# Kernel optimization log

Hardware: AMD Instinct MI355X
Metric: run time of the kernel (lower is better)

Reference implementation:

```python
import jax, jax.numpy as jnp
import numpy as np

B, C, N = 4, 256, 4096
QK = 32  # query/key channel dim hardcoded in module


def setup_inputs() -> dict:
    key = jax.random.key(0)
    ks = jax.random.split(key, 5)
    sc = 1.0 / np.sqrt(C)
    return {
        "x": jax.random.normal(ks[0], (B, C, N), dtype=jnp.float32),
        "Wf": jax.random.normal(ks[1], (QK, C), dtype=jnp.float32) * sc,
        "bf": jnp.zeros((QK,), dtype=jnp.float32),
        "Wg": jax.random.normal(ks[2], (QK, C), dtype=jnp.float32) * sc,
        "bg": jnp.zeros((QK,), dtype=jnp.float32),
        "Wh": jax.random.normal(ks[3], (C, C), dtype=jnp.float32) * sc,
        "bh": jnp.zeros((C,), dtype=jnp.float32),
        "gamma": jax.random.normal(ks[4], (1,), dtype=jnp.float32) * 0.1,
    }


def reference(x, Wf, bf, Wg, bg, Wh, bh, gamma):
    # 1x1 Conv1d == channel-mixing matmul: (O,C) x (B,C,N) -> (B,O,N)
    f = jnp.einsum('oc,bcn->bon', Wf, x) + bf[:, None]   # (B, 32, N)
    g = jnp.einsum('oc,bcn->bon', Wg, x) + bg[:, None]   # (B, 32, N)
    h = jnp.einsum('oc,bcn->bon', Wh, x) + bh[:, None]   # (B, C, N)
    # attention[b, n, m] = sum_k f[b,k,n] * g[b,k,m]  (unscaled, per source)
    attn = jax.nn.softmax(jnp.einsum('bkn,bkm->bnm', f, g), axis=-1)  # (B,N,N)
    # torch.bmm(h, attention): out[b,c,m] = sum_n h[b,c,n] * attn[b,n,m]
    sa = jnp.einsum('bcn,bnm->bcm', h, attn)             # (B, C, N)
    return gamma * sa + x
```

## Files before the change

kernel.cpp:

```cpp
#include <hip/hip_runtime.h>
#include <hip/hip_bf16.h>
#include <math.h>

constexpr int Bb = 4;
constexpr int Cc = 256;
constexpr int Nn = 4096;
constexpr int K  = 32;

constexpr float LOG2E = 1.4426950408889634f;
constexpr float C40L  = 40.0f * LOG2E;

typedef __attribute__((ext_vector_type(8))) short short8;
typedef __attribute__((ext_vector_type(4))) float f32x4;
typedef __attribute__((ext_vector_type(2))) unsigned int uint2v;

static __device__ __forceinline__ unsigned int pack2(float a, float b) {
  union { __hip_bfloat162 h2; unsigned int u; } cv;
  cv.h2 = __float22bfloat162_rn(float2{a, b});
  return cv.u;
}
static __device__ __forceinline__ unsigned short f2bf(float f) {
  union { __hip_bfloat16 h; unsigned short u; } cv;
  cv.h = __float2bfloat16(f);
  return cv.u;
}
static __device__ __forceinline__ f32x4 MF(short8 a, short8 b, f32x4 c) {
  return __builtin_amdgcn_mfma_f32_16x16x32_bf16(a, b, c, 0, 0, 0);
}
static __device__ __forceinline__ float ex2(float v) {
  return __builtin_amdgcn_exp2f(v);
}
static __device__ __forceinline__ void stage16(const unsigned short* g,
                                               unsigned short* l) {
  __builtin_amdgcn_global_load_lds(
      (const __attribute__((address_space(1))) unsigned int*)g,
      (__attribute__((address_space(3))) unsigned int*)l, 16, 0, 0);
}


__global__ __launch_bounds__(256) void castW(
    const float* __restrict__ Wh, unsigned short* __restrict__ Whb)
{
  int i = (blockIdx.x * 256 + threadIdx.x) * 4;
  float4 v = *(const float4*)&Wh[i];
  uint2 o = { pack2(v.x, v.y), pack2(v.z, v.w) };
  *(uint2*)&Whb[i] = o;
}

__global__ __launch_bounds__(256) void castFG(
    const float* __restrict__ Wf, const float* __restrict__ Wg,
    unsigned short* __restrict__ Wfgb)
{
  int g = (blockIdx.x * 256 + threadIdx.x) * 4;
  int row = g >> 8, c = g & 255;
  const float* src = (row < 32) ? &Wf[row*Cc + c] : &Wg[(row-32)*Cc + c];
  float4 v = *(const float4*)src;
  uint2 o = { pack2(v.x, v.y), pack2(v.z, v.w) };
  *(uint2*)&Wfgb[g] = o;
}

__global__ __launch_bounds__(256) void trans_k(
    const float* __restrict__ x, unsigned short* __restrict__ xT)
{
  __shared__ unsigned short Ls[64][65];
  const int b  = blockIdx.z;
  const int n0 = blockIdx.x * 64, c0 = blockIdx.y * 64;
  const int tid = threadIdx.x;
  {
    const int cr = tid >> 4, n4 = (tid & 15) * 4;
#pragma unroll
    for (int rr = 0; rr < 4; ++rr) {
      int c = rr * 16 + cr;
      float4 v = *(const float4*)&x[(size_t)(b*Cc + c0 + c)*Nn + n0 + n4];
      Ls[c][n4+0] = f2bf(v.x); Ls[c][n4+1] = f2bf(v.y);
      Ls[c][n4+2] = f2bf(v.z); Ls[c][n4+3] = f2bf(v.w);
    }
  }
  __syncthreads();
  {
    const int nw = tid >> 4, cw = (tid & 15) * 4;
#pragma unroll
    for (int rr = 0; rr < 4; ++rr) {
      int n = nw + rr * 16;
      unsigned int lo = (unsigned int)Ls[cw+0][n] | ((unsigned int)Ls[cw+1][n] << 16);
      unsigned int hi = (unsigned int)Ls[cw+2][n] | ((unsigned int)Ls[cw+3][n] << 16);
      uint2 o = { lo, hi };
      *(uint2*)&xT[(size_t)(b*Nn + n0 + n)*Cc + c0 + cw] = o;
    }
  }
}

__global__ __launch_bounds__(256) void proj_fgM(
    const unsigned short* __restrict__ xT, const unsigned short* __restrict__ Wfgb,
    const float* __restrict__ bf, const float* __restrict__ bg,
    unsigned short* __restrict__ Ft, unsigned short* __restrict__ Gt)
{
  const int b = blockIdx.y;
  const int tid = threadIdx.x, wave = tid >> 6, lane = tid & 63;
  const int q = lane >> 4, col = lane & 15;
  const int n = blockIdx.x * 64 + wave * 16 + col;

  const unsigned short* Bp = xT + (size_t)(b*Nn + n)*Cc + q*8;
  const f32x4 zero = {0.f,0.f,0.f,0.f};
  f32x4 af0 = zero, af1 = zero, ag0 = zero, ag1 = zero;
#pragma unroll
  for (int kc = 0; kc < 8; ++kc) {
    short8 bn = *(const short8*)(Bp + kc*32);
    short8 a0 = *(const short8*)(Wfgb + (size_t)( 0 + col)*Cc + kc*32 + q*8);
    short8 a1 = *(const short8*)(Wfgb + (size_t)(16 + col)*Cc + kc*32 + q*8);
    short8 a2 = *(const short8*)(Wfgb + (size_t)(32 + col)*Cc + kc*32 + q*8);
    short8 a3 = *(const short8*)(Wfgb + (size_t)(48 + col)*Cc + kc*32 + q*8);
    af0 = MF(a0, bn, af0); af1 = MF(a1, bn, af1);
    ag0 = MF(a2, bn, ag0); ag1 = MF(a3, bn, ag1);
  }
  float4 bf0 = *(const float4*)&bf[q*4],      bf1 = *(const float4*)&bf[16 + q*4];
  float4 bg0 = *(const float4*)&bg[q*4],      bg1 = *(const float4*)&bg[16 + q*4];
  uint2 F0 = { pack2((af0[0]+bf0.x)*LOG2E, (af0[1]+bf0.y)*LOG2E),
               pack2((af0[2]+bf0.z)*LOG2E, (af0[3]+bf0.w)*LOG2E) };
  uint2 F1 = { pack2((af1[0]+bf1.x)*LOG2E, (af1[1]+bf1.y)*LOG2E),
               pack2((af1[2]+bf1.z)*LOG2E, (af1[3]+bf1.w)*LOG2E) };
  uint2 G0 = { pack2(ag0[0]+bg0.x, ag0[1]+bg0.y), pack2(ag0[2]+bg0.z, ag0[3]+bg0.w) };
  uint2 G1 = { pack2(ag1[0]+bg1.x, ag1[1]+bg1.y), pack2(ag1[2]+bg1.z, ag1[3]+bg1.w) };
  unsigned short* fo = Ft + (size_t)(b*Nn + n)*K;
  unsigned short* go = Gt + (size_t)(b*Nn + n)*K;
  *(uint2*)(fo + q*4) = F0;  *(uint2*)(fo + 16 + q*4) = F1;
  *(uint2*)(go + q*4) = G0;  *(uint2*)(go + 16 + q*4) = G1;
}

__global__ __launch_bounds__(512) void pass1(
    const unsigned short* __restrict__ Ft, const unsigned short* __restrict__ Gt,
    unsigned short* __restrict__ Et, float* __restrict__ Lp)
{
  __shared__ float red[8][64];
  const int n0 = blockIdx.x * 64;
  const int mh = blockIdx.y;
  const int b  = blockIdx.z;
  const int tid = threadIdx.x, wave = tid >> 6, lane = tid & 63;
  const int q = lane >> 4, col = lane & 15;
  const unsigned short* Fb = Ft + (size_t)b*Nn*K;
  const unsigned short* Gb = Gt + (size_t)b*Nn*K;
  unsigned short* Ebt = Et + (size_t)b*Nn*Nn;

  short8 af[4];
#pragma unroll
  for (int rb = 0; rb < 4; ++rb)
    af[rb] = *(const short8*)(Fb + (size_t)(n0 + rb*16 + col)*K + q*8);

  const int mw = mh*2048 + wave*256;
  const f32x4 cinit = {-C40L, -C40L, -C40L, -C40L};
  float l[16];
#pragma unroll
  for (int i = 0; i < 16; ++i) l[i] = 0.f;

  unsigned short* sbase = Ebt + (size_t)(n0 >> 3)*128
                        + (q >> 1)*128 + col*8 + (q & 1)*4;

  short8 gA = *(const short8*)(Gb + (size_t)(mw + col)*K + q*8);
  for (int it = 0; it < 16; ++it) {
    short8 gB = *(const short8*)(Gb + (size_t)(mw + ((it+1)&15)*16 + col)*K + q*8);
    f32x4 ts[4];
    ts[0] = MF(af[0], gA, cinit);
    ts[1] = MF(af[1], gA, cinit);
    ts[2] = MF(af[2], gA, cinit);
    ts[3] = MF(af[3], gA, cinit);
    const int mt = (mw >> 4) + it;
    unsigned short* sb = sbase + (size_t)mt * (Nn*16);
#pragma unroll
    for (int rb = 0; rb < 4; ++rb) {
      float e0 = ex2(ts[rb][0]), e1 = ex2(ts[rb][1]);
      float e2 = ex2(ts[rb][2]), e3 = ex2(ts[rb][3]);
      l[rb*4+0] += e0; l[rb*4+1] += e1; l[rb*4+2] += e2; l[rb*4+3] += e3;
      uint2v w = { pack2(e0, e1), pack2(e2, e3) };
      __builtin_nontemporal_store(w, (uint2v*)(sb + rb*256));
    }
    gA = gB;
  }
#pragma unroll
  for (int d = 1; d < 16; d <<= 1) {
#pragma unroll
    for (int i = 0; i < 16; ++i) l[i] += __shfl_xor(l[i], d);
  }
  if (col == 0) {
#pragma unroll
    for (int rb = 0; rb < 4; ++rb) {
      float4 v = {l[rb*4+0], l[rb*4+1], l[rb*4+2], l[rb*4+3]};
      *(float4*)&red[wave][rb*16 + q*4] = v;
    }
  }
  __syncthreads();
  if (tid < 64) {
    float t = 0.f;
#pragma unroll
    for (int w = 0; w < 8; ++w) t += red[w][tid];
    Lp[((size_t)mh*Bb + b)*Nn + n0 + tid] = t;
  }
}

__global__ __launch_bounds__(256) void sumL(
    const float* __restrict__ Lp, float* __restrict__ L)
{
  int i = blockIdx.x * 256 + threadIdx.x;
  L[i] = Lp[i] + Lp[(size_t)Bb*Nn + i];
}

__global__ __launch_bounds__(256) void proj_hT(
    const unsigned short* __restrict__ xT, const unsigned short* __restrict__ Whb,
    const float* __restrict__ bh, const float* __restrict__ L,
    unsigned short* __restrict__ Ht)
{
  const int b   = blockIdx.z;
  const int n0  = blockIdx.x * 64;
  const int c0  = blockIdx.y * 64;
  const int tid = threadIdx.x;
  const int wave = tid >> 6, lane = tid & 63;
  const int q = lane >> 4, col = lane & 15;
  const int nw = n0 + wave * 16;

  const unsigned short* Arow  = xT  + (size_t)(b*Nn + nw + col) * Cc + q*8;
  const unsigned short* Bbase = Whb + (size_t)(c0 + col) * Cc + q*8;

  const f32x4 zero = {0.f,0.f,0.f,0.f};
  f32x4 acc[4] = {zero, zero, zero, zero};

  short8 a0 = *(const short8*)(Arow);
  short8 b0[4], b1[4];
#pragma unroll
  for (int j = 0; j < 4; ++j) b0[j] = *(const short8*)(Bbase + (size_t)(j*16)*Cc);

  for (int ks = 0; ks < 256; ks += 64) {
    int k1 = (ks + 32) & 255;
    short8 a1 = *(const short8*)(Arow + k1);
#pragma unroll
    for (int j = 0; j < 4; ++j) b1[j] = *(const short8*)(Bbase + (size_t)(j*16)*Cc + k1);
#pragma unroll
    for (int j = 0; j < 4; ++j) acc[j] = MF(a0, b0[j], acc[j]);
    int k2 = (ks + 64) & 255;
    a0 = *(const short8*)(Arow + k2);
#pragma unroll
    for (int j = 0; j < 4; ++j) b0[j] = *(const short8*)(Bbase + (size_t)(j*16)*Cc + k2);
#pragma unroll
    for (int j = 0; j < 4; ++j) acc[j] = MF(a1, b1[j], acc[j]);
  }

  float4 lv = *(const float4*)&L[(size_t)b*Nn + nw + q*4];
  float linv[4] = {1.f/lv.x, 1.f/lv.y, 1.f/lv.z, 1.f/lv.w};
  unsigned short* Hbt = Ht + (size_t)b*Cc*Nn;
  unsigned short* wb = Hbt + (size_t)(nw >> 3)*128 + (q >> 1)*128 + col*8 + (q & 1)*4;
#pragma unroll
  for (int j = 0; j < 4; ++j) {
    float bb = bh[c0 + j*16 + col];
    float v0 = (acc[j][0] + bb) * linv[0];
    float v1 = (acc[j][1] + bb) * linv[1];
    float v2 = (acc[j][2] + bb) * linv[2];
    float v3 = (acc[j][3] + bb) * linv[3];
    uint2v w = { pack2(v0, v1), pack2(v2, v3) };
    *(uint2v*)(wb + (size_t)((c0 >> 4) + j) * (Nn*16)) = w;
  }
}

__global__ __launch_bounds__(256) void out_gemm2(
    const unsigned short* __restrict__ Ht, const unsigned short* __restrict__ Et,
    const float* __restrict__ x, const float* __restrict__ gamma,
    float* __restrict__ out)
{
  __shared__ unsigned short As[2][8192];
  __shared__ unsigned short Bs[2][8192];
  constexpr int TS = Nn * 16;

  const int id  = blockIdx.x;
  const int xcd = id & 7, s = id >> 3;
  const int b    = xcd >> 1;
  const int tile = s + (xcd & 1) * 32;
  const int c0 = (tile & 1) * 128;
  const int m0 = (tile >> 1) * 128;
  const int tid = threadIdx.x, wave = tid >> 6, lane = tid & 63;
  const int q = lane >> 4, col = lane & 15;
  const int wc = wave & 1, wm = wave >> 1;

  const unsigned short* Ag = Ht + (size_t)b*Cc*Nn + (size_t)(c0 >> 4)*TS;
  const unsigned short* Bg = Et + (size_t)b*Nn*Nn + (size_t)(m0 >> 4)*TS;

  auto stage = [&](int buf, int k0) {
    const int kb = (k0 >> 3) * 128;
    if (wave < 2) {
      unsigned short* ld = &As[buf][0];
#pragma unroll
      for (int i = 0; i < 8; ++i) {
        int j = wave*8 + i, ct = j >> 1, h2 = j & 1;
        stage16(Ag + (size_t)ct*TS + kb + h2*512 + lane*8,
                ld + ct*1024 + h2*512);
      }
    } else {
      unsigned short* ld = &Bs[buf][0];
#pragma unroll
      for (int i = 0; i < 8; ++i) {
        int j = (wave-2)*8 + i, mt = j >> 1, h2 = j & 1;
        stage16(Bg + (size_t)mt*TS + kb + h2*512 + lane*8,
                ld + mt*1024 + h2*512);
      }
    }
  };

  const f32x4 zero = {0.f,0.f,0.f,0.f};
  f32x4 acc[4][4];
#pragma unroll
  for (int i = 0; i < 4; ++i)
#pragma unroll
    for (int j = 0; j < 4; ++j) acc[i][j] = zero;

  auto compute = [&](int buf) {
#pragma unroll
    for (int kc = 0; kc < 2; ++kc) {
      short8 af[4], ef[4];
#pragma unroll
      for (int i = 0; i < 4; ++i) {
        af[i] = *(const short8*)&As[buf][(wc*4+i)*1024 + (kc*4+q)*128 + col*8];
        ef[i] = *(const short8*)&Bs[buf][(wm*4+i)*1024 + (kc*4+q)*128 + col*8];
      }
#pragma unroll
      for (int ci = 0; ci < 4; ++ci)
#pragma unroll
        for (int mi = 0; mi < 4; ++mi)
          acc[ci][mi] = MF(af[ci], ef[mi], acc[ci][mi]);
    }
  };

  stage(0, 0);
  __syncthreads();
  for (int t = 0; t < 63; ++t) {
    stage((t + 1) & 1, (t + 1) * 64);
    compute(t & 1);
    __syncthreads();
  }
  compute(1);

  const float gm = gamma[0];
#pragma unroll
  for (int ci = 0; ci < 4; ++ci) {
#pragma unroll
    for (int mi = 0; mi < 4; ++mi) {
      const int m = m0 + wm*64 + mi*16 + col;
#pragma unroll
      for (int r = 0; r < 4; ++r) {
        int c = c0 + wc*64 + ci*16 + q*4 + r;
        size_t idx = ((size_t)(b*Cc + c))*Nn + m;
        out[idx] = fmaf(gm, acc[ci][mi][r], x[idx]);
      }
    }
  }
}

__global__ __launch_bounds__(256) void proj_h(
    const unsigned short* __restrict__ xT, const unsigned short* __restrict__ Whb,
    const float* __restrict__ bh, unsigned short* __restrict__ H)
{
  const int b   = blockIdx.z;
  const int n0  = blockIdx.x * 64;
  const int c0  = blockIdx.y * 64;
  const int tid = threadIdx.x;
  const int wave = tid >> 6, lane = tid & 63;
  const int q = lane >> 4, col = lane & 15;
  const int cw = c0 + wave * 16;

  const unsigned short* Arow = Whb + (size_t)(cw + col) * Cc + q*8;
  const unsigned short* Bbase = xT + (size_t)(b*Nn + n0 + col) * Cc + q*8;

  const f32x4 zero = {0.f,0.f,0.f,0.f};
  f32x4 acc[4] = {zero, zero, zero, zero};

  short8 a0 = *(const short8*)(Arow);
  short8 b0[4], b1[4];
#pragma unroll
  for (int j = 0; j < 4; ++j) b0[j] = *(const short8*)(Bbase + (size_t)(j*16)*Cc);

  for (int ks = 0; ks < 256; ks += 64) {
    int k1 = (ks + 32) & 255;
    short8 a1 = *(const short8*)(Arow + k1);
#pragma unroll
    for (int j = 0; j < 4; ++j) b1[j] = *(const short8*)(Bbase + (size_t)(j*16)*Cc + k1);
#pragma unroll
    for (int j = 0; j < 4; ++j) acc[j] = MF(a0, b0[j], acc[j]);
    int k2 = (ks + 64) & 255;
    a0 = *(const short8*)(Arow + k2);
#pragma unroll
    for (int j = 0; j < 4; ++j) b0[j] = *(const short8*)(Bbase + (size_t)(j*16)*Cc + k2);
#pragma unroll
    for (int j = 0; j < 4; ++j) acc[j] = MF(a1, b1[j], acc[j]);
  }

  float4 bb = *(const float4*)&bh[cw + q*4];
  float brs[4] = {bb.x, bb.y, bb.z, bb.w};
#pragma unroll
  for (int j = 0; j < 4; ++j) {
#pragma unroll
    for (int r = 0; r < 4; ++r) {
      int c = cw + q*4 + r;
      int n = n0 + j*16 + col;
      H[(size_t)(b*Cc + c)*Nn + n] = f2bf(acc[j][r] + brs[r]);
    }
  }
}

__global__ __launch_bounds__(256) void stats_k(
    const unsigned short* __restrict__ Ft, const unsigned short* __restrict__ Gt,
    float* __restrict__ Lp)
{
  __shared__ float red[4][32];
  const int b = blockIdx.y >> 1, ms = blockIdx.y & 1;
  const int n0 = blockIdx.x * 32;
  const int tid = threadIdx.x, wave = tid >> 6, lane = tid & 63;
  const int q = lane >> 4, col = lane & 15;
  const unsigned short* Fb = Ft + (size_t)b*Nn*K;
  const unsigned short* Gb = Gt + (size_t)b*Nn*K;

  short8 af0 = *(const short8*)(Fb + (size_t)(n0      + col)*K + q*8);
  short8 af1 = *(const short8*)(Fb + (size_t)(n0 + 16 + col)*K + q*8);
  const int mq = ms*2048 + wave*512;
  const f32x4 zero = {0.f,0.f,0.f,0.f};
  float l[8] = {0.f,0.f,0.f,0.f,0.f,0.f,0.f,0.f};

  short8 gfA = *(const short8*)(Gb + (size_t)(mq + col)*K + q*8);
  for (int it = 0; it < 32; ++it) {
    short8 gfB = *(const short8*)(Gb + (size_t)(mq + ((it+1)&31)*16 + col)*K + q*8);
    f32x4 s0 = MF(af0, gfA, zero);
    f32x4 s1 = MF(af1, gfA, zero);
#pragma unroll
    for (int r = 0; r < 4; ++r) {
      l[r]   += ex2(s0[r] - C40L);
      l[4+r] += ex2(s1[r] - C40L);
    }
    gfA = gfB;
  }
#pragma unroll
  for (int d = 1; d < 16; d <<= 1) {
#pragma unroll
    for (int r = 0; r < 8; ++r) l[r] += __shfl_xor(l[r], d);
  }
  if (col == 0) {
    float4 v0 = {l[0], l[1], l[2], l[3]};
    float4 v1 = {l[4], l[5], l[6], l[7]};
    *(float4*)&red[wave][q*4]      = v0;
    *(float4*)&red[wave][16 + q*4] = v1;
  }
  __syncthreads();
  if (tid < 32) {
    float t = red[0][tid] + red[1][tid] + red[2][tid] + red[3][tid];
    Lp[((size_t)ms*Bb + b)*Nn + n0 + tid] = t;
  }
}

__global__ __launch_bounds__(256) void zcomb(
    const float* __restrict__ Lp, float* __restrict__ Z2)
{
  int i = blockIdx.x * 256 + threadIdx.x;
  Z2[i] = C40L + __log2f(Lp[i] + Lp[(size_t)Bb*Nn + i]);
}

struct Gen { short8 af0, af1; short8 hf[4]; };

__global__ __launch_bounds__(256, 4) void out_k(
    const unsigned short* __restrict__ Ft, const unsigned short* __restrict__ Gt,
    const unsigned short* __restrict__ H, const float* __restrict__ Z2,
    const float* __restrict__ x, const float* __restrict__ gamma,
    float* __restrict__ dst)
{
  __shared__ unsigned short Ps[4][32*40];
  const int b   = blockIdx.y;
  const int m0  = blockIdx.x * 64;
  const int c0b = blockIdx.z * 128;
  const int tid = threadIdx.x, wave = tid >> 6, lane = tid & 63;
  const int q = lane >> 4, col = lane & 15;
  const int mw  = m0 + (wave & 1) * 32;
  const int c0w = c0b + (wave >> 1) * 64;

  const unsigned short* Fb = Ft + (size_t)b*Nn*K;
  const unsigned short* Hb = H  + (size_t)b*Cc*Nn;
  const float*          Zb = Z2 + (size_t)b*Nn;

  short8 gf0 = *(const short8*)(Gt + (size_t)(b*Nn + mw      + col)*K + q*8);
  short8 gf1 = *(const short8*)(Gt + (size_t)(b*Nn + mw + 16 + col)*K + q*8);

  unsigned short* Pw = &Ps[wave][0];
  const f32x4 zero = {0.f,0.f,0.f,0.f};
  f32x4 acc[2][4];
#pragma unroll
  for (int j = 0; j < 2; ++j)
#pragma unroll
    for (int i = 0; i < 4; ++i) acc[j][i] = zero;

  Gen A, B;
  auto loadGen = [&](Gen& G, int nt) {
    G.af0 = *(const short8*)(Fb + (size_t)(nt      + col)*K + q*8);
    G.af1 = *(const short8*)(Fb + (size_t)(nt + 16 + col)*K + q*8);
#pragma unroll
    for (int i = 0; i < 4; ++i)
      G.hf[i] = *(const short8*)(Hb + (size_t)(c0w + i*16 + col)*Nn + nt + q*8);
  };
  auto step = [&](int nt, Gen& CUR, Gen& NXT) {
    loadGen(NXT, (nt + 32) & (Nn - 1));
    float4 z0 = *(const float4*)(Zb + nt + q*4);
    float4 z1 = *(const float4*)(Zb + nt + 16 + q*4);
    f32x4 s00 = MF(CUR.af0, gf0, zero);
    f32x4 s01 = MF(CUR.af0, gf1, zero);
    f32x4 s10 = MF(CUR.af1, gf0, zero);
    f32x4 s11 = MF(CUR.af1, gf1, zero);
    uint2 w00 = { pack2(ex2(s00[0]-z0.x), ex2(s00[1]-z0.y)),
                  pack2(ex2(s00[2]-z0.z), ex2(s00[3]-z0.w)) };
    uint2 w01 = { pack2(ex2(s01[0]-z0.x), ex2(s01[1]-z0.y)),
                  pack2(ex2(s01[2]-z0.z), ex2(s01[3]-z0.w)) };
    uint2 w10 = { pack2(ex2(s10[0]-z1.x), ex2(s10[1]-z1.y)),
                  pack2(ex2(s10[2]-z1.z), ex2(s10[3]-z1.w)) };
    uint2 w11 = { pack2(ex2(s11[0]-z1.x), ex2(s11[1]-z1.y)),
                  pack2(ex2(s11[2]-z1.z), ex2(s11[3]-z1.w)) };
    *(uint2*)&Pw[(     col)*40      + q*4] = w00;
    *(uint2*)&Pw[(16 + col)*40      + q*4] = w01;
    *(uint2*)&Pw[(     col)*40 + 16 + q*4] = w10;
    *(uint2*)&Pw[(16 + col)*40 + 16 + q*4] = w11;
    short8 pf0 = *(const short8*)&Pw[(     col)*40 + q*8];
    short8 pf1 = *(const short8*)&Pw[(16 + col)*40 + q*8];
#pragma unroll
    for (int i = 0; i < 4; ++i) {
      acc[0][i] = MF(CUR.hf[i], pf0, acc[0][i]);
      acc[1][i] = MF(CUR.hf[i], pf1, acc[1][i]);
    }
  };

  loadGen(A, 0);
  for (int t = 0; t < 128; t += 2) {
    step(t*32,      A, B);
    step(t*32 + 32, B, A);
  }

  const float gm = gamma[0];
#pragma unroll
  for (int mj = 0; mj < 2; ++mj) {
    const int m = mw + mj*16 + col;
#pragma unroll
    for (int i = 0; i < 4; ++i) {
#pragma unroll
      for (int r = 0; r < 4; ++r) {
        int c = c0w + i*16 + q*4 + r;
        size_t idx = ((size_t)(b*Cc + c))*Nn + m;
        dst[idx] = fmaf(gm, acc[mj][i][r], x[idx]);
      }
    }
  }
}

extern "C" void kernel_launch(void* const* d_in, const int* in_sizes, int n_in,
                              void* d_out, int out_size, void* d_ws, size_t ws_size,
                              hipStream_t stream) {
  (void)in_sizes; (void)n_in; (void)out_size;
  const float* x     = (const float*)d_in[0];
  const float* Wf    = (const float*)d_in[1];
  const float* bf    = (const float*)d_in[2];
  const float* Wg    = (const float*)d_in[3];
  const float* bg    = (const float*)d_in[4];
  const float* Wh    = (const float*)d_in[5];
  const float* bh    = (const float*)d_in[6];
  const float* gamma = (const float*)d_in[7];
  float* out = (float*)d_out;

  unsigned short* Ft   = (unsigned short*)d_ws;
  unsigned short* Gt   = Ft   + (size_t)Bb*Nn*K;
  unsigned short* xT   = Gt   + (size_t)Bb*Nn*K;
  unsigned short* H    = xT   + (size_t)Bb*Nn*Cc;
  unsigned short* Whb  = H    + (size_t)Bb*Cc*Nn;
  unsigned short* Wfgb = Whb  + (size_t)Cc*Cc;
  float*          L    = (float*)(Wfgb + 64*Cc);
  float*          Z2   = L  + (size_t)Bb*Nn;
  float*          Lp   = Z2 + (size_t)Bb*Nn;
  unsigned short* Et   = (unsigned short*)(Lp + 2*(size_t)Bb*Nn);

  const size_t baseEnd = 19038208ull + 65536ull*4;
  const size_t needE   = baseEnd + (size_t)Bb*Nn*Nn*2;

  castW   <<<dim3(Cc*Cc/1024), 256, 0, stream>>>(Wh, Whb);
  castFG  <<<dim3(64*Cc/1024), 256, 0, stream>>>(Wf, Wg, Wfgb);
  trans_k <<<dim3(Nn/64, Cc/64, Bb), 256, 0, stream>>>(x, xT);
  proj_fgM<<<dim3(Nn/64, Bb), 256, 0, stream>>>(xT, Wfgb, bf, bg, Ft, Gt);

  if (ws_size >= needE) {
    pass1    <<<dim3(Nn/64, 2, Bb), 512, 0, stream>>>(Ft, Gt, Et, Lp);
    sumL     <<<dim3(Bb*Nn/256), 256, 0, stream>>>(Lp, L);
    proj_hT  <<<dim3(Nn/64, Cc/64, Bb), 256, 0, stream>>>(xT, Whb, bh, L, H);
    out_gemm2<<<dim3(256), 256, 0, stream>>>(H, Et, x, gamma, out);
  } else {
    proj_h  <<<dim3(Nn/64, Cc/64, Bb), 256, 0, stream>>>(xT, Whb, bh, H);
    stats_k <<<dim3(Nn/32, 2*Bb), 256, 0, stream>>>(Ft, Gt, Lp);
    zcomb   <<<dim3(Bb*Nn/256), 256, 0, stream>>>(Lp, Z2);
    out_k   <<<dim3(Nn/64, Bb, 2), 256, 0, stream>>>(Ft, Gt, H, Z2, x, gamma, out);
  }
}
```

Before: 224.8 us.

## Split out_gemm K dimension four ways with atomic accumulation into pre-initialized output

The final H·E GEMM now splits the n-reduction into four chunks, launching 1024 blocks instead of 256 with half-size LDS tiles and a launch bound of 4 blocks per CU. Partial sums are atomically added into out, which a new initX kernel first fills with x. Gamma is folded into the H projection scaling so the epilogue needs no extra multiply. This trades better occupancy and load balance across CUs for float atomics, an extra pass over out, and non-deterministic summation order.

```diff
diff --git a/kernel.cpp b/kernel.cpp
--- a/kernel.cpp
+++ b/kernel.cpp
@@ -206,7 +206,7 @@
 __global__ __launch_bounds__(256) void proj_hT(
     const unsigned short* __restrict__ xT, const unsigned short* __restrict__ Whb,
     const float* __restrict__ bh, const float* __restrict__ L,
-    unsigned short* __restrict__ Ht)
+    const float* __restrict__ gamma, unsigned short* __restrict__ Ht)
 {
   const int b   = blockIdx.z;
   const int n0  = blockIdx.x * 64;
@@ -242,8 +242,9 @@
     for (int j = 0; j < 4; ++j) acc[j] = MF(a1, b1[j], acc[j]);
   }
 
+  const float gm = gamma[0];
   float4 lv = *(const float4*)&L[(size_t)b*Nn + nw + q*4];
-  float linv[4] = {1.f/lv.x, 1.f/lv.y, 1.f/lv.z, 1.f/lv.w};
+  float linv[4] = {gm/lv.x, gm/lv.y, gm/lv.z, gm/lv.w};
   unsigned short* Hbt = Ht + (size_t)b*Cc*Nn;
   unsigned short* wb = Hbt + (size_t)(nw >> 3)*128 + (q >> 1)*128 + col*8 + (q & 1)*4;
 #pragma unroll
@@ -258,45 +259,54 @@
   }
 }
 
-__global__ __launch_bounds__(256) void out_gemm2(
+__global__ __launch_bounds__(256) void initX(
+    const float* __restrict__ x, float* __restrict__ out)
+{
+  size_t i = ((size_t)blockIdx.x * 256 + threadIdx.x) * 4;
+  float4 v = *(const float4*)&x[i];
+  *(float4*)&out[i] = v;
+}
+
+__global__ __launch_bounds__(256, 4) void out_gemm3(
     const unsigned short* __restrict__ Ht, const unsigned short* __restrict__ Et,
-    const float* __restrict__ x, const float* __restrict__ gamma,
     float* __restrict__ out)
 {
-  __shared__ unsigned short As[2][8192];
-  __shared__ unsigned short Bs[2][8192];
+  __shared__ unsigned short As[2][4096];
+  __shared__ unsigned short Bs[2][4096];
   constexpr int TS = Nn * 16;
 
-  const int id  = blockIdx.x;
-  const int xcd = id & 7, s = id >> 3;
-  const int b    = xcd >> 1;
-  const int tile = s + (xcd & 1) * 32;
-  const int c0 = (tile & 1) * 128;
-  const int m0 = (tile >> 1) * 128;
+  const int id = blockIdx.x;
+  const int ct = id >> 9;
+  const int r  = id & 511;
+  const int mt = r >> 4;
+  const int b  = (r >> 2) & 3;
+  const int ks = r & 3;
+  const int c0 = ct * 128;
+  const int m0 = mt * 128;
+  const int nb16 = ks * 16384;
+
   const int tid = threadIdx.x, wave = tid >> 6, lane = tid & 63;
   const int q = lane >> 4, col = lane & 15;
   const int wc = wave & 1, wm = wave >> 1;
 
-  const unsigned short* Ag = Ht + (size_t)b*Cc*Nn + (size_t)(c0 >> 4)*TS;
-  const unsigned short* Bg = Et + (size_t)b*Nn*Nn + (size_t)(m0 >> 4)*TS;
-
-  auto stage = [&](int buf, int k0) {
-    const int kb = (k0 >> 3) * 128;
+  const unsigned short* Ag = Ht + (size_t)b*Cc*Nn + (size_t)(c0 >> 4)*TS + nb16;
+  const unsigned short* Bg = Et + (size_t)b*Nn*Nn + (size_t)(m0 >> 4)*TS + nb16;
+
+  auto stage = [&](int buf, int t) {
+    const int kb = t * 512;
     if (wave < 2) {
       unsigned short* ld = &As[buf][0];
 #pragma unroll
-      for (int i = 0; i < 8; ++i) {
-        int j = wave*8 + i, ct = j >> 1, h2 = j & 1;
-        stage16(Ag + (size_t)ct*TS + kb + h2*512 + lane*8,
-                ld + ct*1024 + h2*512);
+      for (int i = 0; i < 4; ++i) {
+        int ct8 = wave*4 + i;
+        stage16(Ag + (size_t)ct8*TS + kb + lane*8, ld + ct8*512);
       }
     } else {
       unsigned short* ld = &Bs[buf][0];
 #pragma unroll
-      for (int i = 0; i < 8; ++i) {
-        int j = (wave-2)*8 + i, mt = j >> 1, h2 = j & 1;
-        stage16(Bg + (size_t)mt*TS + kb + h2*512 + lane*8,
-                ld + mt*1024 + h2*512);
+      for (int i = 0; i < 4; ++i) {
+        int mt8 = (wave-2)*4 + i;
+        stage16(Bg + (size_t)mt8*TS + kb + lane*8, ld + mt8*512);
       }
     }
   };
@@ -309,42 +319,37 @@
     for (int j = 0; j < 4; ++j) acc[i][j] = zero;
 
   auto compute = [&](int buf) {
-#pragma unroll
-    for (int kc = 0; kc < 2; ++kc) {
-      short8 af[4], ef[4];
-#pragma unroll
-      for (int i = 0; i < 4; ++i) {
-        af[i] = *(const short8*)&As[buf][(wc*4+i)*1024 + (kc*4+q)*128 + col*8];
-        ef[i] = *(const short8*)&Bs[buf][(wm*4+i)*1024 + (kc*4+q)*128 + col*8];
-      }
-#pragma unroll
-      for (int ci = 0; ci < 4; ++ci)
-#pragma unroll
-        for (int mi = 0; mi < 4; ++mi)
-          acc[ci][mi] = MF(af[ci], ef[mi], acc[ci][mi]);
-    }
+    short8 af[4], ef[4];
+#pragma unroll
+    for (int i = 0; i < 4; ++i) {
+      af[i] = *(const short8*)&As[buf][(wc*4+i)*512 + q*128 + col*8];
+      ef[i] = *(const short8*)&Bs[buf][(wm*4+i)*512 + q*128 + col*8];
+    }
+#pragma unroll
+    for (int ci = 0; ci < 4; ++ci)
+#pragma unroll
+      for (int mi = 0; mi < 4; ++mi)
+        acc[ci][mi] = MF(af[ci], ef[mi], acc[ci][mi]);
   };
 
   stage(0, 0);
   __syncthreads();
-  for (int t = 0; t < 63; ++t) {
-    stage((t + 1) & 1, (t + 1) * 64);
+  for (int t = 0; t < 31; ++t) {
+    stage((t + 1) & 1, t + 1);
     compute(t & 1);
     __syncthreads();
   }
   compute(1);
 
-  const float gm = gamma[0];
 #pragma unroll
   for (int ci = 0; ci < 4; ++ci) {
 #pragma unroll
     for (int mi = 0; mi < 4; ++mi) {
       const int m = m0 + wm*64 + mi*16 + col;
 #pragma unroll
-      for (int r = 0; r < 4; ++r) {
-        int c = c0 + wc*64 + ci*16 + q*4 + r;
-        size_t idx = ((size_t)(b*Cc + c))*Nn + m;
-        out[idx] = fmaf(gm, acc[ci][mi][r], x[idx]);
+      for (int rr = 0; rr < 4; ++rr) {
+        int c = c0 + wc*64 + ci*16 + q*4 + rr;
+        atomicAdd(&out[((size_t)(b*Cc + c))*Nn + m], acc[ci][mi][rr]);
       }
     }
   }
@@ -583,8 +588,9 @@
   if (ws_size >= needE) {
     pass1    <<<dim3(Nn/64, 2, Bb), 512, 0, stream>>>(Ft, Gt, Et, Lp);
     sumL     <<<dim3(Bb*Nn/256), 256, 0, stream>>>(Lp, L);
-    proj_hT  <<<dim3(Nn/64, Cc/64, Bb), 256, 0, stream>>>(xT, Whb, bh, L, H);
-    out_gemm2<<<dim3(256), 256, 0, stream>>>(H, Et, x, gamma, out);
+    proj_hT  <<<dim3(Nn/64, Cc/64, Bb), 256, 0, stream>>>(xT, Whb, bh, L, gamma, H);
+    initX    <<<dim3((size_t)Bb*Cc*Nn/1024), 256, 0, stream>>>(x, out);
+    out_gemm3<<<dim3(1024), 256, 0, stream>>>(H, Et, out);
   } else {
     proj_h  <<<dim3(Nn/64, Cc/64, Bb), 256, 0, stream>>>(xT, Whb, bh, H);
     stats_k <<<dim3(Nn/32, 2*Bb), 256, 0, stream>>>(Ft, Gt, Lp);
```

Result: slower. 235.1 us (+4.6%).
